# Performance work log

Hardware: AMD Instinct MI355X
Metric: run time of the kernel (lower is better)

Reference implementation:

```python
import jax, jax.numpy as jnp
import numpy as np

D_HEAD = 64  # module's self.heads scaling constant


def setup_inputs() -> dict:
    key = jax.random.key(0)
    kq, kk, kv = jax.random.split(key, 3)
    N, HW, C = 4, 4096, 64
    Q = jax.random.normal(kq, (N, HW, C), dtype=jnp.float32)
    K = jax.random.normal(kk, (N, HW, C), dtype=jnp.float32)
    V = jax.random.normal(kv, (N, HW, C), dtype=jnp.float32)
    return {"Q": Q, "K": K, "V": V}


def reference(Q, K, V):
    # logits[n, q, k] = Q[n,q,:] . K[n,k,:] / sqrt(d_head)
    scale = 1.0 / jnp.sqrt(jnp.asarray(D_HEAD, dtype=Q.dtype))
    logits = jnp.einsum("nqc,nkc->nqk", Q, K) * scale  # [N, HW, HW]
    # NOTE: softmax over the QUERY axis (dim=1), non-standard
    attn = jax.nn.softmax(logits, axis=1)
    return jnp.einsum("nqk,nkc->nqc", attn, V)
```

## Files before the change

### kernel.cpp

```cpp
#include <hip/hip_runtime.h>

#define NB 4
#define HWN 4096
#define CD 64
#define NSTRIDE (HWN * CD)

typedef short short8 __attribute__((ext_vector_type(8), may_alias));
typedef short short4v __attribute__((ext_vector_type(4), may_alias));
typedef float f32x4 __attribute__((ext_vector_type(4), may_alias));

__device__ constexpr float C1 = 0.18033688011112042f;

__device__ __forceinline__ unsigned short f2bf(float f) {
    unsigned u = __builtin_bit_cast(unsigned, f);
    u = (u + 0x7FFFu + ((u >> 16) & 1u)) >> 16;
    return (unsigned short)u;
}

__device__ __forceinline__ float fexp2(float x) {
#if __has_builtin(__builtin_amdgcn_exp2f)
    return __builtin_amdgcn_exp2f(x);
#else
    return exp2f(x);
#endif
}

__device__ __forceinline__ size_t qk_swz(int row, int c) {
    return (size_t)(row >> 4) * 1024 + (c >> 5) * 512 +
           ((((c >> 3) & 3) * 16 + (row & 15)) * 8) + (c & 7);
}

__global__ __launch_bounds__(256) void cvt_qk(const float* __restrict__ Q,
                                              const float* __restrict__ K,
                                              unsigned short* __restrict__ Qs,
                                              unsigned short* __restrict__ Ks) {
    int i = (blockIdx.x * 256 + threadIdx.x) * 4;
    int rg = i >> 6, c = i & 63;
    int n = rg >> 12, r = rg & 4095;
    float4 q = *(const float4*)(Q + i);
    float4 k = *(const float4*)(K + i);
    ushort4 qo, ko;
    qo.x = f2bf(q.x * C1); qo.y = f2bf(q.y * C1);
    qo.z = f2bf(q.z * C1); qo.w = f2bf(q.w * C1);
    ko.x = f2bf(k.x); ko.y = f2bf(k.y); ko.z = f2bf(k.z); ko.w = f2bf(k.w);
    size_t off = (size_t)n * NSTRIDE + qk_swz(r, c);
    *(ushort4*)(Qs + off) = qo;
    *(ushort4*)(Ks + off) = ko;
}

__global__ __attribute__((amdgpu_flat_work_group_size(256, 256), amdgpu_waves_per_eu(2, 4)))
void lsum_kernel(const unsigned short* __restrict__ Qs,
                 const unsigned short* __restrict__ Ks,
                 float* __restrict__ l) {
    int tid = threadIdx.x;
    int w = tid >> 6, lane = tid & 63, quad = lane >> 4, m16 = lane & 15;
    int n = blockIdx.y;
    int kbase = blockIdx.x * 256 + w * 64;

    const unsigned short* Kp = Ks + (size_t)n * NSTRIDE + (kbase >> 4) * 1024 + lane * 8;
    short8 ka0 = *(const short8*)(Kp);
    short8 ka1 = *(const short8*)(Kp + 512);
    short8 kb0 = *(const short8*)(Kp + 1024);
    short8 kb1 = *(const short8*)(Kp + 1536);
    short8 kc0 = *(const short8*)(Kp + 2048);
    short8 kc1 = *(const short8*)(Kp + 2560);
    short8 kd0 = *(const short8*)(Kp + 3072);
    short8 kd1 = *(const short8*)(Kp + 3584);

    const unsigned short* Qp = Qs + (size_t)n * NSTRIDE + blockIdx.z * 16384 + lane * 8;

    short8 qc0 = *(const short8*)(Qp);
    short8 qc1 = *(const short8*)(Qp + 512);
    Qp += 1024;

    float lA[4] = {0.f, 0.f, 0.f, 0.f};
    float lB[4] = {0.f, 0.f, 0.f, 0.f};
    float lC[4] = {0.f, 0.f, 0.f, 0.f};
    float lD[4] = {0.f, 0.f, 0.f, 0.f};
#pragma unroll 2
    for (int qc = 0; qc < 16; ++qc) {
        short8 qn0 = *(const short8*)(Qp);
        short8 qn1 = *(const short8*)(Qp + 512);
        f32x4 a = {0.f, 0.f, 0.f, 0.f}, b = a, c = a, d = a;
        a = __builtin_amdgcn_mfma_f32_16x16x32_bf16(ka0, qc0, a, 0, 0, 0);
        a = __builtin_amdgcn_mfma_f32_16x16x32_bf16(ka1, qc1, a, 0, 0, 0);
        b = __builtin_amdgcn_mfma_f32_16x16x32_bf16(kb0, qc0, b, 0, 0, 0);
        b = __builtin_amdgcn_mfma_f32_16x16x32_bf16(kb1, qc1, b, 0, 0, 0);
        c = __builtin_amdgcn_mfma_f32_16x16x32_bf16(kc0, qc0, c, 0, 0, 0);
        c = __builtin_amdgcn_mfma_f32_16x16x32_bf16(kc1, qc1, c, 0, 0, 0);
        d = __builtin_amdgcn_mfma_f32_16x16x32_bf16(kd0, qc0, d, 0, 0, 0);
        d = __builtin_amdgcn_mfma_f32_16x16x32_bf16(kd1, qc1, d, 0, 0, 0);
#pragma unroll
        for (int r = 0; r < 4; ++r) {
            lA[r] += fexp2(a[r]);
            lB[r] += fexp2(b[r]);
            lC[r] += fexp2(c[r]);
            lD[r] += fexp2(d[r]);
        }
        qc0 = qn0; qc1 = qn1;
        Qp += 1024;
    }
#pragma unroll
    for (int r = 0; r < 4; ++r)
        for (int d1 = 1; d1 < 16; d1 <<= 1) {
            lA[r] += __shfl_xor(lA[r], d1);
            lB[r] += __shfl_xor(lB[r], d1);
            lC[r] += __shfl_xor(lC[r], d1);
            lD[r] += __shfl_xor(lD[r], d1);
        }
    if (m16 == 0) {
        float* lp = l + n * HWN + kbase + quad * 4;
#pragma unroll
        for (int r = 0; r < 4; ++r) {
            atomicAdd(lp + r, lA[r]);
            atomicAdd(lp + 16 + r, lB[r]);
            atomicAdd(lp + 32 + r, lC[r]);
            atomicAdd(lp + 48 + r, lD[r]);
        }
    }
}

__global__ __launch_bounds__(256) void prep_v(const float* __restrict__ V,
                                              const float* __restrict__ l,
                                              unsigned short* __restrict__ Vts) {
    __shared__ float rl[64];
    __shared__ float tile[64][65];
    int tid = threadIdx.x, n = blockIdx.y, kbase = blockIdx.x * 64;
    if (tid < 64) rl[tid] = 1.0f / l[n * HWN + kbase + tid];
    __syncthreads();
#pragma unroll
    for (int i = 0; i < 16; ++i) {
        int e = i * 256 + tid;
        int k = e >> 6, c = e & 63;
        tile[c][k] = V[((size_t)(n * HWN + kbase + k)) * CD + c] * rl[k];
    }
    __syncthreads();
#pragma unroll
    for (int i = 0; i < 2; ++i) {
        int s = i * 256 + tid;
        int kb32 = s >> 8;
        int ct = (s >> 6) & 3;
        int ll = s & 63;
        int cc = ct * 16 + (ll & 15);
        int kq = ((ll >> 4) & 3) * 4;
        int k0 = kb32 * 32 + kq;
        short8 v;
#pragma unroll
        for (int j = 0; j < 4; ++j) {
            v[j]     = (short)f2bf(tile[cc][k0 + j]);
            v[4 + j] = (short)f2bf(tile[cc][k0 + 16 + j]);
        }
        size_t off = (size_t)n * NSTRIDE + (size_t)((kbase >> 5) + kb32) * 2048 +
                     ct * 512 + ll * 8;
        *(short8*)(Vts + off) = v;
    }
}

__global__ __attribute__((amdgpu_flat_work_group_size(256, 256), amdgpu_waves_per_eu(2, 4)))
void attn_kernel(const unsigned short* __restrict__ Qs,
                 const unsigned short* __restrict__ Ks,
                 const unsigned short* __restrict__ Vts,
                 float* __restrict__ partial,
                 int nit) {
    int tid = threadIdx.x;
    int w = tid >> 6, lane = tid & 63, quad = lane >> 4, m16 = lane & 15;
    int n = blockIdx.y;
    int qbase = blockIdx.x * 64 + w * 16;

    const unsigned short* Qp = Qs + (size_t)n * NSTRIDE + (qbase >> 4) * 1024 + lane * 8;
    short8 qf0 = *(const short8*)(Qp);
    short8 qf1 = *(const short8*)(Qp + 512);

    size_t kofs = (size_t)blockIdx.z * (size_t)nit * 2048;
    const unsigned short* Kp = Ks + (size_t)n * NSTRIDE + kofs + lane * 8;
    const unsigned short* Vp = Vts + (size_t)n * NSTRIDE + kofs + lane * 8;

    f32x4 o[4];
#pragma unroll
    for (int ct = 0; ct < 4; ++ct) o[ct] = f32x4{0.f, 0.f, 0.f, 0.f};

#pragma unroll 2
    for (int it = 0; it < nit; ++it) {
        short8 kf00 = *(const short8*)(Kp);
        short8 kf01 = *(const short8*)(Kp + 512);
        short8 kf10 = *(const short8*)(Kp + 1024);
        short8 kf11 = *(const short8*)(Kp + 1536);
        f32x4 sA = {0.f, 0.f, 0.f, 0.f}, sB = sA;
        sA = __builtin_amdgcn_mfma_f32_16x16x32_bf16(kf00, qf0, sA, 0, 0, 0);
        sA = __builtin_amdgcn_mfma_f32_16x16x32_bf16(kf01, qf1, sA, 0, 0, 0);
        sB = __builtin_amdgcn_mfma_f32_16x16x32_bf16(kf10, qf0, sB, 0, 0, 0);
        sB = __builtin_amdgcn_mfma_f32_16x16x32_bf16(kf11, qf1, sB, 0, 0, 0);

        short4v pA, pB;
#pragma unroll
        for (int r = 0; r < 4; ++r) {
            pA[r] = (short)f2bf(fexp2(sA[r]));
            pB[r] = (short)f2bf(fexp2(sB[r]));
        }

#pragma unroll
        for (int ct = 0; ct < 4; ++ct) {
            short8 vf = *(const short8*)(Vp + ct * 512);
            short4v vlo = __builtin_shufflevector(vf, vf, 0, 1, 2, 3);
            short4v vhi = __builtin_shufflevector(vf, vf, 4, 5, 6, 7);
            o[ct] = __builtin_amdgcn_mfma_f32_16x16x16bf16_1k(vlo, pA, o[ct], 0, 0, 0);
            o[ct] = __builtin_amdgcn_mfma_f32_16x16x16bf16_1k(vhi, pB, o[ct], 0, 0, 0);
        }
        Kp += 2048;
        Vp += 2048;
    }

    float* pp = partial + (size_t)blockIdx.z * (NB * HWN * CD) +
                ((size_t)(n * HWN + qbase + m16)) * CD + quad * 4;
#pragma unroll
    for (int ct = 0; ct < 4; ++ct)
        *(f32x4*)(pp + ct * 16) = o[ct];
}

__global__ __launch_bounds__(256) void reduce_out(const float* __restrict__ p,
                                                  float* __restrict__ out, int ns) {
    int i = (blockIdx.x * 256 + threadIdx.x) * 4;
    f32x4 a = *(const f32x4*)(p + i);
    for (int s = 1; s < ns; ++s)
        a = a + *(const f32x4*)(p + (size_t)s * (NB * HWN * CD) + i);
    *(f32x4*)(out + i) = a;
}

extern "C" void kernel_launch(void* const* d_in, const int* in_sizes, int n_in,
                              void* d_out, int out_size, void* d_ws, size_t ws_size,
                              hipStream_t stream) {
    const float* Q = (const float*)d_in[0];
    const float* K = (const float*)d_in[1];
    const float* V = (const float*)d_in[2];
    float* out = (float*)d_out;

    char* ws = (char*)d_ws;
    unsigned short* Qs  = (unsigned short*)(ws);
    unsigned short* Ks  = (unsigned short*)(ws + (1u << 21));
    unsigned short* Vts = (unsigned short*)(ws + (2u << 21));
    float* l       = (float*)(ws + (3u << 21));
    float* partial = (float*)(ws + (4u << 21));

    size_t base = (size_t)(4u << 21);
    size_t slice = (size_t)NB * HWN * CD * sizeof(float);
    int ns = (ws_size >= base + 4 * slice) ? 4 : 2;
    int nit = HWN / ns / 32;

    (void)hipMemsetAsync(l, 0, (size_t)NB * HWN * sizeof(float), stream);

    cvt_qk<<<1024, 256, 0, stream>>>(Q, K, Qs, Ks);
    lsum_kernel<<<dim3(16, NB, 16), 256, 0, stream>>>(Qs, Ks, l);
    prep_v<<<dim3(64, NB), 256, 0, stream>>>(V, l, Vts);
    attn_kernel<<<dim3(64, NB, ns), 256, 0, stream>>>(Qs, Ks, Vts, partial, nit);
    reduce_out<<<1024, 256, 0, stream>>>(partial, out, ns);
}
```

Baseline: 123.0 us.

## Process two query tiles per wave to reuse K/V loads, raise key split

Each wave now handles 32 queries (two 16-row tiles) instead of 16, so every K and V fragment loaded from memory feeds twice as many MFMAs. The grid's query dimension is halved, and the key-axis split is raised to 8 when the workspace allows it, to keep enough blocks in flight. The exp results are packed with the packed float2-to-bf16 conversion intrinsic instead of per-element manual rounding. The costs are higher register pressure and more partial slices for reduce_out to read and sum.

```diff
diff --git a/kernel.cpp b/kernel.cpp
--- a/kernel.cpp
+++ b/kernel.cpp
@@ -1,4 +1,5 @@
 #include <hip/hip_runtime.h>
+#include <hip/hip_bf16.h>
 
 #define NB 4
 #define HWN 4096
@@ -23,6 +24,13 @@
 #else
     return exp2f(x);
 #endif
+}
+
+__device__ __forceinline__ unsigned pk2(float a, float b) {
+    __hip_bfloat162 h = __float22bfloat162_rn(float2{a, b});
+    unsigned u;
+    __builtin_memcpy(&u, &h, 4);
+    return u;
 }
 
 __device__ __forceinline__ size_t qk_swz(int row, int c) {
@@ -165,19 +173,21 @@
     int tid = threadIdx.x;
     int w = tid >> 6, lane = tid & 63, quad = lane >> 4, m16 = lane & 15;
     int n = blockIdx.y;
-    int qbase = blockIdx.x * 64 + w * 16;
+    int qbase = blockIdx.x * 128 + w * 16;
 
     const unsigned short* Qp = Qs + (size_t)n * NSTRIDE + (qbase >> 4) * 1024 + lane * 8;
-    short8 qf0 = *(const short8*)(Qp);
-    short8 qf1 = *(const short8*)(Qp + 512);
+    short8 qa0 = *(const short8*)(Qp);
+    short8 qa1 = *(const short8*)(Qp + 512);
+    short8 qb0 = *(const short8*)(Qp + 4096);
+    short8 qb1 = *(const short8*)(Qp + 4096 + 512);
 
     size_t kofs = (size_t)blockIdx.z * (size_t)nit * 2048;
     const unsigned short* Kp = Ks + (size_t)n * NSTRIDE + kofs + lane * 8;
     const unsigned short* Vp = Vts + (size_t)n * NSTRIDE + kofs + lane * 8;
 
-    f32x4 o[4];
-#pragma unroll
-    for (int ct = 0; ct < 4; ++ct) o[ct] = f32x4{0.f, 0.f, 0.f, 0.f};
+    f32x4 oA[4], oB[4];
+#pragma unroll
+    for (int ct = 0; ct < 4; ++ct) { oA[ct] = f32x4{0.f, 0.f, 0.f, 0.f}; oB[ct] = oA[ct]; }
 
 #pragma unroll 2
     for (int it = 0; it < nit; ++it) {
@@ -185,36 +195,48 @@
         short8 kf01 = *(const short8*)(Kp + 512);
         short8 kf10 = *(const short8*)(Kp + 1024);
         short8 kf11 = *(const short8*)(Kp + 1536);
-        f32x4 sA = {0.f, 0.f, 0.f, 0.f}, sB = sA;
-        sA = __builtin_amdgcn_mfma_f32_16x16x32_bf16(kf00, qf0, sA, 0, 0, 0);
-        sA = __builtin_amdgcn_mfma_f32_16x16x32_bf16(kf01, qf1, sA, 0, 0, 0);
-        sB = __builtin_amdgcn_mfma_f32_16x16x32_bf16(kf10, qf0, sB, 0, 0, 0);
-        sB = __builtin_amdgcn_mfma_f32_16x16x32_bf16(kf11, qf1, sB, 0, 0, 0);
-
-        short4v pA, pB;
-#pragma unroll
-        for (int r = 0; r < 4; ++r) {
-            pA[r] = (short)f2bf(fexp2(sA[r]));
-            pB[r] = (short)f2bf(fexp2(sB[r]));
-        }
+        f32x4 s00 = {0.f, 0.f, 0.f, 0.f}, s01 = s00, s10 = s00, s11 = s00;
+        s00 = __builtin_amdgcn_mfma_f32_16x16x32_bf16(kf00, qa0, s00, 0, 0, 0);
+        s00 = __builtin_amdgcn_mfma_f32_16x16x32_bf16(kf01, qa1, s00, 0, 0, 0);
+        s01 = __builtin_amdgcn_mfma_f32_16x16x32_bf16(kf10, qa0, s01, 0, 0, 0);
+        s01 = __builtin_amdgcn_mfma_f32_16x16x32_bf16(kf11, qa1, s01, 0, 0, 0);
+        s10 = __builtin_amdgcn_mfma_f32_16x16x32_bf16(kf00, qb0, s10, 0, 0, 0);
+        s10 = __builtin_amdgcn_mfma_f32_16x16x32_bf16(kf01, qb1, s10, 0, 0, 0);
+        s11 = __builtin_amdgcn_mfma_f32_16x16x32_bf16(kf10, qb0, s11, 0, 0, 0);
+        s11 = __builtin_amdgcn_mfma_f32_16x16x32_bf16(kf11, qb1, s11, 0, 0, 0);
+
+        uint2 w00, w01, w10, w11;
+        w00.x = pk2(fexp2(s00[0]), fexp2(s00[1])); w00.y = pk2(fexp2(s00[2]), fexp2(s00[3]));
+        w01.x = pk2(fexp2(s01[0]), fexp2(s01[1])); w01.y = pk2(fexp2(s01[2]), fexp2(s01[3]));
+        w10.x = pk2(fexp2(s10[0]), fexp2(s10[1])); w10.y = pk2(fexp2(s10[2]), fexp2(s10[3]));
+        w11.x = pk2(fexp2(s11[0]), fexp2(s11[1])); w11.y = pk2(fexp2(s11[2]), fexp2(s11[3]));
+        short4v pA0 = __builtin_bit_cast(short4v, w00);
+        short4v pA1 = __builtin_bit_cast(short4v, w01);
+        short4v pB0 = __builtin_bit_cast(short4v, w10);
+        short4v pB1 = __builtin_bit_cast(short4v, w11);
 
 #pragma unroll
         for (int ct = 0; ct < 4; ++ct) {
             short8 vf = *(const short8*)(Vp + ct * 512);
             short4v vlo = __builtin_shufflevector(vf, vf, 0, 1, 2, 3);
             short4v vhi = __builtin_shufflevector(vf, vf, 4, 5, 6, 7);
-            o[ct] = __builtin_amdgcn_mfma_f32_16x16x16bf16_1k(vlo, pA, o[ct], 0, 0, 0);
-            o[ct] = __builtin_amdgcn_mfma_f32_16x16x16bf16_1k(vhi, pB, o[ct], 0, 0, 0);
+            oA[ct] = __builtin_amdgcn_mfma_f32_16x16x16bf16_1k(vlo, pA0, oA[ct], 0, 0, 0);
+            oA[ct] = __builtin_amdgcn_mfma_f32_16x16x16bf16_1k(vhi, pA1, oA[ct], 0, 0, 0);
+            oB[ct] = __builtin_amdgcn_mfma_f32_16x16x16bf16_1k(vlo, pB0, oB[ct], 0, 0, 0);
+            oB[ct] = __builtin_amdgcn_mfma_f32_16x16x16bf16_1k(vhi, pB1, oB[ct], 0, 0, 0);
         }
         Kp += 2048;
         Vp += 2048;
     }
 
-    float* pp = partial + (size_t)blockIdx.z * (NB * HWN * CD) +
-                ((size_t)(n * HWN + qbase + m16)) * CD + quad * 4;
-#pragma unroll
-    for (int ct = 0; ct < 4; ++ct)
-        *(f32x4*)(pp + ct * 16) = o[ct];
+    float* ppA = partial + (size_t)blockIdx.z * (NB * HWN * CD) +
+                 ((size_t)(n * HWN + qbase + m16)) * CD + quad * 4;
+    float* ppB = ppA + (size_t)64 * CD;
+#pragma unroll
+    for (int ct = 0; ct < 4; ++ct) {
+        *(f32x4*)(ppA + ct * 16) = oA[ct];
+        *(f32x4*)(ppB + ct * 16) = oB[ct];
+    }
 }
 
 __global__ __launch_bounds__(256) void reduce_out(const float* __restrict__ p,
@@ -243,7 +265,8 @@
 
     size_t base = (size_t)(4u << 21);
     size_t slice = (size_t)NB * HWN * CD * sizeof(float);
-    int ns = (ws_size >= base + 4 * slice) ? 4 : 2;
+    int ns = (ws_size >= base + 8 * slice) ? 8
+           : (ws_size >= base + 4 * slice) ? 4 : 2;
     int nit = HWN / ns / 32;
 
     (void)hipMemsetAsync(l, 0, (size_t)NB * HWN * sizeof(float), stream);
@@ -251,6 +274,6 @@
     cvt_qk<<<1024, 256, 0, stream>>>(Q, K, Qs, Ks);
     lsum_kernel<<<dim3(16, NB, 16), 256, 0, stream>>>(Qs, Ks, l);
     prep_v<<<dim3(64, NB), 256, 0, stream>>>(V, l, Vts);
-    attn_kernel<<<dim3(64, NB, ns), 256, 0, stream>>>(Qs, Ks, Vts, partial, nit);
+    attn_kernel<<<dim3(32, NB, ns), 256, 0, stream>>>(Qs, Ks, Vts, partial, nit);
     reduce_out<<<1024, 256, 0, stream>>>(partial, out, ns);
 }
```

Measured after the change: 111.7 us. 9.2% less time.
